# Optimization experiments

Hardware: AMD Instinct MI355X
Metric: run time of the kernel (lower is better)

The kernel has to match this reference:

```python
import jax, jax.numpy as jnp
import numpy as np

NUM_HEADS = 8
MAX_REL = 32  # max_relative_positions
LN_EPS = 1e-5


def _conv1x1(x, W, b):
    # x: (B, C, H, W), W: (Cout, Cin), b: (Cout,)
    return jnp.einsum('bchw,oc->bohw', x, W) + b[None, :, None, None]


def setup_inputs() -> dict:
    key = jax.random.key(0)
    ks = jax.random.split(key, 10)
    B, C, H, W = 2, 512, 48, 48
    L = H * W
    s = 1.0 / np.sqrt(C)
    inp = {
        'x': jax.random.normal(ks[0], (B, C, H, W), jnp.float32),
        'mask': jax.random.randint(ks[1], (1, NUM_HEADS, L, L), 0, 2).astype(bool),
        'learnable_pos': jax.random.normal(ks[2], (1, C, H, W), jnp.float32) * 0.02,
        'Wq': jax.random.normal(ks[3], (C, C), jnp.float32) * s,
        'bq': jnp.zeros((C,), jnp.float32),
        'Wk': jax.random.normal(ks[4], (C, C), jnp.float32) * s,
        'bk': jnp.zeros((C,), jnp.float32),
        'Wv': jax.random.normal(ks[5], (C, C), jnp.float32) * s,
        'bv': jnp.zeros((C,), jnp.float32),
        'Wo': jax.random.normal(ks[6], (C, C), jnp.float32) * s,
        'bo': jnp.zeros((C,), jnp.float32),
        'rel_table': jax.random.normal(ks[7], (NUM_HEADS, 2 * MAX_REL + 1), jnp.float32) * 0.02,
        'ln_gamma': jnp.ones((C,), jnp.float32),
        'ln_beta': jnp.zeros((C,), jnp.float32),
    }
    return inp


def reference(x, mask, learnable_pos, Wq, bq, Wk, bk, Wv, bv, Wo, bo,
              rel_table, ln_gamma, ln_beta):
    B, C, H, W = x.shape
    L = H * W
    hd = C // NUM_HEADS
    residual = x

    xp = x + learnable_pos
    q = _conv1x1(xp, Wq, bq)
    k = _conv1x1(xp, Wk, bk)
    v = _conv1x1(xp, Wv, bv)

    def split_heads(t):  # (B,C,H,W) -> (B, heads, L, hd)
        return t.reshape(B, NUM_HEADS, hd, L).transpose(0, 1, 3, 2)

    q, k, v = split_heads(q), split_heads(k), split_heads(v)

    scale = 1.0 / np.sqrt(hd).astype(np.float32)
    scores = jnp.einsum('bhld,bhmd->bhlm', q, k) * scale  # (B,H,L,L)

    # relative positional bias per head
    pos = jnp.arange(L)
    rp = jnp.clip(pos[:, None] - pos[None, :], -MAX_REL, MAX_REL) + MAX_REL  # (L,L)
    scores = scores + rel_table[:, rp][None]  # (1,heads,L,L) broadcast

    scores = jnp.where(mask, scores, jnp.float32(-1e9))
    attn = jax.nn.softmax(scores, axis=-1)

    out = jnp.einsum('bhlm,bhmd->bhld', attn, v)  # (B,heads,L,hd)
    out = out.transpose(0, 1, 3, 2).reshape(B, C, H, W)
    out = _conv1x1(out, Wo, bo)

    y = residual + out
    # LayerNorm over channels (channels-last permute in original)
    yl = y.transpose(0, 2, 3, 1)  # (B,H,W,C)
    mu = jnp.mean(yl, axis=-1, keepdims=True)
    var = jnp.var(yl, axis=-1, keepdims=True)
    yl = (yl - mu) * jax.lax.rsqrt(var + LN_EPS) * ln_gamma + ln_beta
    return yl.transpose(0, 3, 1, 2)
```

## Files before the change

### kernel.cpp

```cpp
#include <hip/hip_runtime.h>
#include <cstdint>

#define L_SEQ 2304
#define CDIM  512
#define NHEADS 8
#define HD    64
#define LL    ((size_t)L_SEQ * L_SEQ)
#define ROWS_TOT (16 * L_SEQ)
#define PERBL ((size_t)2 * L_SEQ * 512)

typedef short  s8v  __attribute__((ext_vector_type(8)));
typedef float  f4v  __attribute__((ext_vector_type(4)));

__device__ __forceinline__ ushort f2bf(float f) {
    union { float f; uint32_t u; } v; v.f = f;
    uint32_t u = v.u;
    uint32_t r = (u + 0x7FFFu + ((u >> 16) & 1u)) >> 16;
    return (ushort)r;
}

__device__ __forceinline__ float bf2f(ushort u) {
    union { uint32_t u; float f; } v; v.u = (uint32_t)u << 16;
    return v.f;
}

__global__ __launch_bounds__(256) void prep_w(
    const float* __restrict__ Wq, const float* __restrict__ Wk,
    const float* __restrict__ Wv, const float* __restrict__ Wo,
    ushort* __restrict__ wb)
{
    const int i   = blockIdx.x * 256 + threadIdx.x;
    const int mat = i >> 16;
    const int j   = i & 65535;
    const float* src = (mat == 0) ? Wq : (mat == 1) ? Wk : (mat == 2) ? Wv : Wo;
    const float4 w = ((const float4*)src)[j];
    ushort4 o;
    o.x = f2bf(w.x); o.y = f2bf(w.y); o.z = f2bf(w.z); o.w = f2bf(w.w);
    ((ushort4*)(wb + (size_t)mat * 262144))[j] = o;
}

__global__ __launch_bounds__(256) void xpose(
    const float* __restrict__ x, const float* __restrict__ pos,
    ushort* __restrict__ xt)
{
    __shared__ ushort T[64][72];
    const int l0 = blockIdx.x * 64;
    const int c0 = blockIdx.y * 64;
    const int b  = blockIdx.z;
    const int t  = threadIdx.x;
    const int cc = t >> 2;
    const int l4 = (t & 3) * 16;
    const size_t off  = ((size_t)b * CDIM + c0 + cc) * L_SEQ + l0 + l4;
    const size_t poff = (size_t)(c0 + cc) * L_SEQ + l0 + l4;
    #pragma unroll
    for (int j4 = 0; j4 < 4; j4++) {
        const float4 xv = *(const float4*)&x[off + j4 * 4];
        const float4 pv = *(const float4*)&pos[poff + j4 * 4];
        T[cc][l4 + j4 * 4 + 0] = f2bf(xv.x + pv.x);
        T[cc][l4 + j4 * 4 + 1] = f2bf(xv.y + pv.y);
        T[cc][l4 + j4 * 4 + 2] = f2bf(xv.z + pv.z);
        T[cc][l4 + j4 * 4 + 3] = f2bf(xv.w + pv.w);
    }
    __syncthreads();
    const int lr = t >> 2;
    const int c4 = (t & 3) * 16;
    ushort o[16];
    #pragma unroll
    for (int j = 0; j < 16; j++) o[j] = T[c4 + j][lr];
    ushort* dst = &xt[((size_t)b * L_SEQ + l0 + lr) * 512 + c0 + c4];
    *(ushort4*)&dst[0]  = *(ushort4*)&o[0];
    *(ushort4*)&dst[4]  = *(ushort4*)&o[4];
    *(ushort4*)&dst[8]  = *(ushort4*)&o[8];
    *(ushort4*)&dst[12] = *(ushort4*)&o[12];
}

__global__ __launch_bounds__(256) void qkv_mfma(
    const ushort* __restrict__ xt, const ushort* __restrict__ wb,
    const float* __restrict__ bq, const float* __restrict__ bk,
    const float* __restrict__ bv,
    ushort* __restrict__ q_t, ushort* __restrict__ k_t, ushort* __restrict__ v_t)
{
    __shared__ __align__(16) ushort Bs[3][1024 * 8];
    const int l0  = blockIdx.x * 64;
    const int o0  = blockIdx.y * 64;
    const int b   = blockIdx.z;
    const int t = threadIdx.x, w = t >> 6, lane = t & 63;
    const int n16 = lane & 15, q4 = lane >> 4;

    const ushort* A = xt + ((size_t)b * L_SEQ + l0 + w * 16 + n16) * 512 + q4 * 8;

    s8v areg[16];
    #pragma unroll
    for (int i = 0; i < 16; i++) areg[i] = *(const s8v*)&A[i * 32];

    int sOff[4];
    #pragma unroll
    for (int i = 0; i < 4; i++) {
        const int c  = t + 256 * i;
        const int fr = c >> 6, ln = c & 63;
        sOff[i] = (o0 + (fr & 3) * 16 + (ln & 15)) * 512 + (fr >> 2) * 32 + (ln >> 4) * 8;
    }

    s8v breg[3][4];
    #pragma unroll
    for (int m = 0; m < 3; m++)
        #pragma unroll
        for (int i = 0; i < 4; i++)
            breg[m][i] = *(const s8v*)&wb[(size_t)m * 262144 + sOff[i]];

    f4v acc[3][4] = {};
    for (int kb = 0; kb < 512; kb += 128) {
        __syncthreads();
        #pragma unroll
        for (int m = 0; m < 3; m++)
            #pragma unroll
            for (int i = 0; i < 4; i++)
                *(s8v*)&Bs[m][(t + 256 * i) * 8] = breg[m][i];
        __syncthreads();
        if (kb < 384) {
            #pragma unroll
            for (int m = 0; m < 3; m++)
                #pragma unroll
                for (int i = 0; i < 4; i++)
                    breg[m][i] = *(const s8v*)&wb[(size_t)m * 262144 + sOff[i] + kb + 128];
        }
        #pragma unroll
        for (int ks = 0; ks < 4; ks++) {
            const s8v a = areg[(kb >> 5) + ks];
            #pragma unroll
            for (int m = 0; m < 3; m++)
                #pragma unroll
                for (int t4 = 0; t4 < 4; t4++) {
                    const s8v bf = *(const s8v*)&Bs[m][((ks * 4 + t4) * 64 + lane) * 8];
                    acc[m][t4] = __builtin_amdgcn_mfma_f32_16x16x32_bf16(a, bf, acc[m][t4], 0, 0, 0);
                }
        }
    }

    const int h = o0 >> 6;
    const int rowbase = l0 + w * 16 + q4 * 4;

    #pragma unroll
    for (int m = 0; m < 2; m++) {
        const float* bias = (m == 0) ? bq : bk;
        const float sc = (m == 0) ? 0.125f : 1.0f;
        ushort* op = (m == 0 ? q_t : k_t) + ((size_t)(b * NHEADS + h)) * L_SEQ * HD;
        #pragma unroll
        for (int t4 = 0; t4 < 4; t4++) {
            const float bi = bias[o0 + t4 * 16 + n16];
            #pragma unroll
            for (int r = 0; r < 4; r++)
                op[(size_t)(rowbase + r) * HD + t4 * 16 + n16] = f2bf((acc[m][t4][r] + bi) * sc);
        }
    }
    {
        ushort* op = v_t + ((size_t)(b * NHEADS + h)) * HD * L_SEQ;
        #pragma unroll
        for (int t4 = 0; t4 < 4; t4++) {
            const float bi = bv[o0 + t4 * 16 + n16];
            ushort4 st;
            st.x = f2bf(acc[2][t4][0] + bi);
            st.y = f2bf(acc[2][t4][1] + bi);
            st.z = f2bf(acc[2][t4][2] + bi);
            st.w = f2bf(acc[2][t4][3] + bi);
            *(ushort4*)&op[(size_t)(t4 * 16 + n16) * L_SEQ + rowbase] = st;
        }
    }
}

__global__ __launch_bounds__(256) void flash_attn_mfma(
    const ushort* __restrict__ q, const ushort* __restrict__ k,
    const ushort* __restrict__ vt, const int* __restrict__ mask,
    const float* __restrict__ rel_table, ushort* __restrict__ Opart,
    float* __restrict__ Lpart)
{
    __shared__ __align__(16) ushort Kf[512 * 8];
    __shared__ __align__(16) ushort Vf[512 * 8];
    __shared__ __align__(16) ushort Pb[4 * 16 * 72];
    __shared__ float rt[65];

    const int t    = threadIdx.x;
    const int id   = blockIdx.x;
    const int h    = id & 7;
    const int s2   = id >> 3;
    const int b    = s2 & 1;
    const int half = (s2 >> 1) & 1;
    const int qb   = s2 >> 2;
    const int bh   = b * NHEADS + h;
    const int l0   = qb * 64;
    const int w    = t >> 6;
    const int lane = t & 63;
    const int n16  = lane & 15;
    const int q4   = lane >> 4;

    if (t < 65) rt[t] = rel_table[h * 65 + t];

    const ushort* qp = q  + (size_t)bh * L_SEQ * HD;
    const ushort* kp = k  + (size_t)bh * L_SEQ * HD;
    const ushort* vp = vt + (size_t)bh * HD * L_SEQ;
    const int*    mp = mask + (size_t)h * LL;

    const int qrow = l0 + w * 16 + n16;
    const s8v qA0 = *(const s8v*)&qp[(size_t)qrow * HD + q4 * 8];
    const s8v qA1 = *(const s8v*)&qp[(size_t)qrow * HD + 32 + q4 * 8];

    f4v O[4] = {{0.f,0.f,0.f,0.f},{0.f,0.f,0.f,0.f},{0.f,0.f,0.f,0.f},{0.f,0.f,0.f,0.f}};
    float lrun[4] = {0.f, 0.f, 0.f, 0.f};

    int sKey[2], sD0[2], sDd[2];
    #pragma unroll
    for (int cc = 0; cc < 2; cc++) {
        const int c = t + cc * 256;
        const int g = c >> 6;
        const int sT = g >> 1, sS = g & 1;
        const int sQ = (c >> 4) & 3, sN = c & 15;
        sKey[cc] = sT * 16 + sN;
        sD0[cc]  = sS * 32 + sQ * 8;
        sDd[cc]  = sT * 16 + sN;
    }

    const int rowbase = l0 + w * 16 + q4 * 4;
    const int kbase = half * 1152;

    s8v kreg[2], vreg[2];
    int mreg[4][4];
    #pragma unroll
    for (int cc = 0; cc < 2; cc++) {
        kreg[cc] = *(const s8v*)&kp[(size_t)(kbase + sKey[cc]) * HD + sD0[cc]];
        vreg[cc] = *(const s8v*)&vp[(size_t)sDd[cc] * L_SEQ + kbase + sD0[cc]];
    }
    #pragma unroll
    for (int t4 = 0; t4 < 4; t4++)
        #pragma unroll
        for (int r = 0; r < 4; r++)
            mreg[t4][r] = mp[(size_t)(rowbase + r) * L_SEQ + kbase + t4 * 16 + n16];

    for (int mt = 0; mt < 18; mt++) {
        const int mb = kbase + mt * 64;
        __syncthreads();
        #pragma unroll
        for (int cc = 0; cc < 2; cc++) {
            const int c = t + cc * 256;
            *(s8v*)&Kf[c * 8] = kreg[cc];
            *(s8v*)&Vf[c * 8] = vreg[cc];
        }
        __syncthreads();

        const int mb2 = (mt < 17) ? mb + 64 : mb;
        s8v knx[2], vnx[2];
        int mnx[4][4];
        #pragma unroll
        for (int cc = 0; cc < 2; cc++) {
            knx[cc] = *(const s8v*)&kp[(size_t)(mb2 + sKey[cc]) * HD + sD0[cc]];
            vnx[cc] = *(const s8v*)&vp[(size_t)sDd[cc] * L_SEQ + mb2 + sD0[cc]];
        }
        #pragma unroll
        for (int t4 = 0; t4 < 4; t4++)
            #pragma unroll
            for (int r = 0; r < 4; r++)
                mnx[t4][r] = mp[(size_t)(rowbase + r) * L_SEQ + mb2 + t4 * 16 + n16];

        f4v S[4];
        #pragma unroll
        for (int t4 = 0; t4 < 4; t4++) {
            const s8v b0 = *(const s8v*)&Kf[((t4 * 2 + 0) * 64 + lane) * 8];
            const s8v b1 = *(const s8v*)&Kf[((t4 * 2 + 1) * 64 + lane) * 8];
            f4v acc = {0.f, 0.f, 0.f, 0.f};
            acc = __builtin_amdgcn_mfma_f32_16x16x32_bf16(qA0, b0, acc, 0, 0, 0);
            acc = __builtin_amdgcn_mfma_f32_16x16x32_bf16(qA1, b1, acc, 0, 0, 0);
            S[t4] = acc;
        }

        #pragma unroll
        for (int t4 = 0; t4 < 4; t4++) {
            const int A = (l0 + w * 16) - (mb + t4 * 16);
            if (A >= 47) {
                const float bu = rt[64];
                #pragma unroll
                for (int r = 0; r < 4; r++) S[t4][r] += bu;
            } else if (A <= -47) {
                const float bu = rt[0];
                #pragma unroll
                for (int r = 0; r < 4; r++) S[t4][r] += bu;
            } else {
                #pragma unroll
                for (int r = 0; r < 4; r++) {
                    int dix = A + q4 * 4 + r - n16;
                    dix = min(max(dix, -32), 32) + 32;
                    S[t4][r] += rt[dix];
                }
            }
            #pragma unroll
            for (int r = 0; r < 4; r++)
                if (mreg[t4][r] == 0) S[t4][r] = -1e9f;
        }

        float sum[4] = {0.f, 0.f, 0.f, 0.f};
        #pragma unroll
        for (int r = 0; r < 4; r++) {
            #pragma unroll
            for (int t4 = 0; t4 < 4; t4++) {
                const float p = __expf(S[t4][r]);
                sum[r] += p;
                Pb[w * 1152 + (q4 * 4 + r) * 72 + t4 * 16 + n16] = f2bf(p);
            }
        }

        const s8v pf0 = *(const s8v*)&Pb[w * 1152 + n16 * 72 + q4 * 8];
        const s8v pf1 = *(const s8v*)&Pb[w * 1152 + n16 * 72 + 32 + q4 * 8];
        #pragma unroll
        for (int t4 = 0; t4 < 4; t4++) {
            f4v o = O[t4];
            const s8v v0 = *(const s8v*)&Vf[((t4 * 2 + 0) * 64 + lane) * 8];
            const s8v v1 = *(const s8v*)&Vf[((t4 * 2 + 1) * 64 + lane) * 8];
            o = __builtin_amdgcn_mfma_f32_16x16x32_bf16(pf0, v0, o, 0, 0, 0);
            o = __builtin_amdgcn_mfma_f32_16x16x32_bf16(pf1, v1, o, 0, 0, 0);
            O[t4] = o;
        }

        #pragma unroll
        for (int r = 0; r < 4; r++) {
            float s = sum[r];
            s += __shfl_xor(s, 1);
            s += __shfl_xor(s, 2);
            s += __shfl_xor(s, 4);
            s += __shfl_xor(s, 8);
            lrun[r] += s;
        }

        #pragma unroll
        for (int cc = 0; cc < 2; cc++) { kreg[cc] = knx[cc]; vreg[cc] = vnx[cc]; }
        #pragma unroll
        for (int t4 = 0; t4 < 4; t4++)
            #pragma unroll
            for (int r = 0; r < 4; r++)
                mreg[t4][r] = mnx[t4][r];
    }

    ushort* op = Opart + (size_t)half * PERBL + (size_t)b * L_SEQ * 512;
    #pragma unroll
    for (int r = 0; r < 4; r++) {
        const size_t base = (size_t)(rowbase + r) * 512 + h * 64;
        #pragma unroll
        for (int t4 = 0; t4 < 4; t4++)
            op[base + t4 * 16 + n16] = f2bf(O[t4][r]);
    }
    if (n16 == 0) {
        const size_t sb = (size_t)half * ROWS_TOT + (size_t)bh * L_SEQ;
        #pragma unroll
        for (int r = 0; r < 4; r++)
            Lpart[sb + rowbase + r] = lrun[r];
    }
}

__global__ __launch_bounds__(256) void combine_kernel(
    const ushort* __restrict__ O01, const float* __restrict__ Lp,
    ushort* __restrict__ at)
{
    const int i   = blockIdx.x * 256 + threadIdx.x;
    const int c8  = i & 63;
    const int row = i >> 6;
    const int b   = row / L_SEQ;
    const int l   = row - b * L_SEQ;
    const int h   = c8 >> 3;
    const size_t s = (size_t)(b * NHEADS + h) * L_SEQ + l;
    const float f = 1.0f / (Lp[s] + Lp[ROWS_TOT + s]);
    const size_t o = (size_t)row * 512 + c8 * 8;
    const ushort4 a0 = *(const ushort4*)&O01[o];
    const ushort4 a1 = *(const ushort4*)&O01[o + 4];
    const ushort4 c0 = *(const ushort4*)&O01[PERBL + o];
    const ushort4 c1 = *(const ushort4*)&O01[PERBL + o + 4];
    ushort4 r0, r1;
    r0.x = f2bf((bf2f(a0.x) + bf2f(c0.x)) * f);
    r0.y = f2bf((bf2f(a0.y) + bf2f(c0.y)) * f);
    r0.z = f2bf((bf2f(a0.z) + bf2f(c0.z)) * f);
    r0.w = f2bf((bf2f(a0.w) + bf2f(c0.w)) * f);
    r1.x = f2bf((bf2f(a1.x) + bf2f(c1.x)) * f);
    r1.y = f2bf((bf2f(a1.y) + bf2f(c1.y)) * f);
    r1.z = f2bf((bf2f(a1.z) + bf2f(c1.z)) * f);
    r1.w = f2bf((bf2f(a1.w) + bf2f(c1.w)) * f);
    *(ushort4*)&at[o]     = r0;
    *(ushort4*)&at[o + 4] = r1;
}

__global__ __launch_bounds__(256) void out_mfma(
    const ushort* __restrict__ at, const ushort* __restrict__ wb,
    const float* __restrict__ bo, const float* __restrict__ x,
    float* __restrict__ y)
{
    __shared__ __align__(16) ushort Bs[1024 * 8];
    const int l0 = blockIdx.x * 64;
    const int o0 = blockIdx.y * 64;
    const int b  = blockIdx.z;
    const int t = threadIdx.x, w = t >> 6, lane = t & 63;
    const int n16 = lane & 15, q4 = lane >> 4;

    const ushort* A = at + ((size_t)b * L_SEQ + l0 + w * 16 + n16) * 512 + q4 * 8;
    const ushort* W = wb + (size_t)3 * 262144;

    s8v areg[16];
    #pragma unroll
    for (int i = 0; i < 16; i++) areg[i] = *(const s8v*)&A[i * 32];

    int sOff[4];
    #pragma unroll
    for (int i = 0; i < 4; i++) {
        const int c  = t + 256 * i;
        const int fr = c >> 6, ln = c & 63;
        sOff[i] = (o0 + (fr & 3) * 16 + (ln & 15)) * 512 + (fr >> 2) * 32 + (ln >> 4) * 8;
    }

    s8v breg[4];
    #pragma unroll
    for (int i = 0; i < 4; i++) breg[i] = *(const s8v*)&W[sOff[i]];

    f4v acc[4] = {{0.f,0.f,0.f,0.f},{0.f,0.f,0.f,0.f},{0.f,0.f,0.f,0.f},{0.f,0.f,0.f,0.f}};
    for (int kb = 0; kb < 512; kb += 128) {
        __syncthreads();
        #pragma unroll
        for (int i = 0; i < 4; i++)
            *(s8v*)&Bs[(t + 256 * i) * 8] = breg[i];
        __syncthreads();
        if (kb < 384) {
            #pragma unroll
            for (int i = 0; i < 4; i++)
                breg[i] = *(const s8v*)&W[sOff[i] + kb + 128];
        }
        #pragma unroll
        for (int ks = 0; ks < 4; ks++) {
            const s8v a = areg[(kb >> 5) + ks];
            #pragma unroll
            for (int t4 = 0; t4 < 4; t4++) {
                const s8v bf = *(const s8v*)&Bs[((ks * 4 + t4) * 64 + lane) * 8];
                acc[t4] = __builtin_amdgcn_mfma_f32_16x16x32_bf16(a, bf, acc[t4], 0, 0, 0);
            }
        }
    }

    const int rowbase = l0 + w * 16 + q4 * 4;
    #pragma unroll
    for (int t4 = 0; t4 < 4; t4++) {
        const int o = o0 + t4 * 16 + n16;
        const float bi = bo[o];
        const size_t off = ((size_t)b * CDIM + o) * L_SEQ + rowbase;
        const float4 xv = *(const float4*)&x[off];
        float4 st;
        st.x = acc[t4][0] + bi + xv.x;
        st.y = acc[t4][1] + bi + xv.y;
        st.z = acc[t4][2] + bi + xv.z;
        st.w = acc[t4][3] + bi + xv.w;
        *(float4*)&y[off] = st;
    }
}

__global__ __launch_bounds__(256) void ln_kernel(
    float* __restrict__ y, const float* __restrict__ gamma,
    const float* __restrict__ beta)
{
    const int t = threadIdx.x;
    const int p = t & 31;
    const int g = t >> 5;
    const int pos = blockIdx.x * 32 + p;
    const int b = (pos >= L_SEQ) ? 1 : 0;
    const int l = pos - b * L_SEQ;
    float* col = y + (size_t)b * CDIM * L_SEQ + l;

    float s = 0.f, sq = 0.f;
    for (int c = g * 64; c < g * 64 + 64; c++) {
        const float v = col[(size_t)c * L_SEQ];
        s += v; sq += v * v;
    }
    __shared__ float S1[8][32];
    __shared__ float S2[8][32];
    S1[g][p] = s; S2[g][p] = sq;
    __syncthreads();
    if (t < 32) {
        float ss = 0.f, qq = 0.f;
        #pragma unroll
        for (int gg = 0; gg < 8; gg++) { ss += S1[gg][t]; qq += S2[gg][t]; }
        const float mu = ss * (1.0f / CDIM);
        const float var = qq * (1.0f / CDIM) - mu * mu;
        S1[0][t] = mu;
        S2[0][t] = rsqrtf(var + 1e-5f);
    }
    __syncthreads();
    const float mu = S1[0][p];
    const float rs = S2[0][p];
    for (int c = g * 64; c < g * 64 + 64; c++) {
        const float v = col[(size_t)c * L_SEQ];
        col[(size_t)c * L_SEQ] = (v - mu) * rs * gamma[c] + beta[c];
    }
}

extern "C" void kernel_launch(void* const* d_in, const int* in_sizes, int n_in,
                              void* d_out, int out_size, void* d_ws, size_t ws_size,
                              hipStream_t stream) {
    const float* x    = (const float*)d_in[0];
    const int* mask   = (const int*)d_in[1];
    const float* pos  = (const float*)d_in[2];
    const float* Wq   = (const float*)d_in[3];
    const float* bq   = (const float*)d_in[4];
    const float* Wk   = (const float*)d_in[5];
    const float* bk   = (const float*)d_in[6];
    const float* Wv   = (const float*)d_in[7];
    const float* bv   = (const float*)d_in[8];
    const float* Wo   = (const float*)d_in[9];
    const float* bo   = (const float*)d_in[10];
    const float* rel  = (const float*)d_in[11];
    const float* gam  = (const float*)d_in[12];
    const float* bet  = (const float*)d_in[13];

    ushort* qw  = (ushort*)d_ws;
    ushort* kw  = qw + PERBL;
    ushort* vw  = kw + PERBL;
    ushort* xtw = vw + PERBL;
    ushort* wbw = xtw + PERBL;
    ushort* Opart = wbw + (size_t)4 * 262144;
    float* Lpart = (float*)(Opart + 2 * PERBL);
    ushort* attnT = xtw;
    float* y = (float*)d_out;

    prep_w<<<dim3(1024), 256, 0, stream>>>(Wq, Wk, Wv, Wo, wbw);

    xpose<<<dim3(L_SEQ / 64, CDIM / 64, 2), 256, 0, stream>>>(x, pos, xtw);

    qkv_mfma<<<dim3(L_SEQ / 64, CDIM / 64, 2), 256, 0, stream>>>(
        xtw, wbw, bq, bk, bv, qw, kw, vw);

    flash_attn_mfma<<<dim3(1152), 256, 0, stream>>>(qw, kw, vw, mask, rel,
                                                    Opart, Lpart);

    combine_kernel<<<dim3(1152), 256, 0, stream>>>(Opart, Lpart, attnT);

    out_mfma<<<dim3(L_SEQ / 64, CDIM / 64, 2), 256, 0, stream>>>(
        attnT, wbw, bo, x, y);

    ln_kernel<<<(2 * L_SEQ) / 32, 256, 0, stream>>>(y, gam, bet);
}
```

Baseline: 369.4 us.

## Pre-swizzle weights into MFMA fragment layout and read B operands directly from global

prep_w now writes the bf16 weights already arranged in per-lane MFMA fragment order, with each thread converting 8 elements. The QKV and output projection kernels drop their LDS staging, the double-buffered register prefetch and the __syncthreads, and load B fragments straight from global memory with coalesced 16-byte loads per k-step. This removes LDS traffic and barriers, but the weight loads now sit inside the MFMA loop without explicit prefetch and depend on L2/cache hits for latency hiding.

```diff
diff --git a/kernel.cpp b/kernel.cpp
--- a/kernel.cpp
+++ b/kernel.cpp
@@ -27,16 +27,23 @@
 __global__ __launch_bounds__(256) void prep_w(
     const float* __restrict__ Wq, const float* __restrict__ Wk,
     const float* __restrict__ Wv, const float* __restrict__ Wo,
-    ushort* __restrict__ wb)
-{
-    const int i   = blockIdx.x * 256 + threadIdx.x;
-    const int mat = i >> 16;
-    const int j   = i & 65535;
+    ushort* __restrict__ wf)
+{
+    const int i    = blockIdx.x * 256 + threadIdx.x;
+    const int lane = i & 63;
+    const int F    = (i >> 6) & 63;
+    const int ob   = (i >> 12) & 7;
+    const int mat  = i >> 15;
     const float* src = (mat == 0) ? Wq : (mat == 1) ? Wk : (mat == 2) ? Wv : Wo;
-    const float4 w = ((const float4*)src)[j];
-    ushort4 o;
-    o.x = f2bf(w.x); o.y = f2bf(w.y); o.z = f2bf(w.z); o.w = f2bf(w.w);
-    ((ushort4*)(wb + (size_t)mat * 262144))[j] = o;
+    const int row = ob * 64 + (F & 3) * 16 + (lane & 15);
+    const int col = (F >> 2) * 32 + (lane >> 4) * 8;
+    const float4 w0 = *(const float4*)&src[(size_t)row * 512 + col];
+    const float4 w1 = *(const float4*)&src[(size_t)row * 512 + col + 4];
+    ushort4 o0, o1;
+    o0.x = f2bf(w0.x); o0.y = f2bf(w0.y); o0.z = f2bf(w0.z); o0.w = f2bf(w0.w);
+    o1.x = f2bf(w1.x); o1.y = f2bf(w1.y); o1.z = f2bf(w1.z); o1.w = f2bf(w1.w);
+    *(ushort4*)&wf[(size_t)i * 8]     = o0;
+    *(ushort4*)&wf[(size_t)i * 8 + 4] = o1;
 }
 
 __global__ __launch_bounds__(256) void xpose(
@@ -75,15 +82,15 @@
 }
 
 __global__ __launch_bounds__(256) void qkv_mfma(
-    const ushort* __restrict__ xt, const ushort* __restrict__ wb,
+    const ushort* __restrict__ xt, const ushort* __restrict__ wf,
     const float* __restrict__ bq, const float* __restrict__ bk,
     const float* __restrict__ bv,
     ushort* __restrict__ q_t, ushort* __restrict__ k_t, ushort* __restrict__ v_t)
 {
-    __shared__ __align__(16) ushort Bs[3][1024 * 8];
-    const int l0  = blockIdx.x * 64;
-    const int o0  = blockIdx.y * 64;
-    const int b   = blockIdx.z;
+    const int l0 = blockIdx.x * 64;
+    const int ob = blockIdx.y;
+    const int o0 = ob * 64;
+    const int b  = blockIdx.z;
     const int t = threadIdx.x, w = t >> 6, lane = t & 63;
     const int n16 = lane & 15, q4 = lane >> 4;
 
@@ -93,51 +100,26 @@
     #pragma unroll
     for (int i = 0; i < 16; i++) areg[i] = *(const s8v*)&A[i * 32];
 
-    int sOff[4];
-    #pragma unroll
-    for (int i = 0; i < 4; i++) {
-        const int c  = t + 256 * i;
-        const int fr = c >> 6, ln = c & 63;
-        sOff[i] = (o0 + (fr & 3) * 16 + (ln & 15)) * 512 + (fr >> 2) * 32 + (ln >> 4) * 8;
-    }
-
-    s8v breg[3][4];
-    #pragma unroll
-    for (int m = 0; m < 3; m++)
-        #pragma unroll
-        for (int i = 0; i < 4; i++)
-            breg[m][i] = *(const s8v*)&wb[(size_t)m * 262144 + sOff[i]];
+    const size_t lb = (size_t)lane * 8;
 
     f4v acc[3][4] = {};
-    for (int kb = 0; kb < 512; kb += 128) {
-        __syncthreads();
+    for (int ks = 0; ks < 16; ks++) {
+        s8v bf[3][4];
         #pragma unroll
         for (int m = 0; m < 3; m++)
             #pragma unroll
-            for (int i = 0; i < 4; i++)
-                *(s8v*)&Bs[m][(t + 256 * i) * 8] = breg[m][i];
-        __syncthreads();
-        if (kb < 384) {
-            #pragma unroll
-            for (int m = 0; m < 3; m++)
-                #pragma unroll
-                for (int i = 0; i < 4; i++)
-                    breg[m][i] = *(const s8v*)&wb[(size_t)m * 262144 + sOff[i] + kb + 128];
-        }
-        #pragma unroll
-        for (int ks = 0; ks < 4; ks++) {
-            const s8v a = areg[(kb >> 5) + ks];
-            #pragma unroll
-            for (int m = 0; m < 3; m++)
-                #pragma unroll
-                for (int t4 = 0; t4 < 4; t4++) {
-                    const s8v bf = *(const s8v*)&Bs[m][((ks * 4 + t4) * 64 + lane) * 8];
-                    acc[m][t4] = __builtin_amdgcn_mfma_f32_16x16x32_bf16(a, bf, acc[m][t4], 0, 0, 0);
-                }
-        }
-    }
-
-    const int h = o0 >> 6;
+            for (int t4 = 0; t4 < 4; t4++)
+                bf[m][t4] = *(const s8v*)&wf[
+                    ((size_t)((m * 8 + ob) * 64 + ks * 4 + t4)) * 512 + lb];
+        const s8v a = areg[ks];
+        #pragma unroll
+        for (int m = 0; m < 3; m++)
+            #pragma unroll
+            for (int t4 = 0; t4 < 4; t4++)
+                acc[m][t4] = __builtin_amdgcn_mfma_f32_16x16x32_bf16(a, bf[m][t4], acc[m][t4], 0, 0, 0);
+    }
+
+    const int h = ob;
     const int rowbase = l0 + w * 16 + q4 * 4;
 
     #pragma unroll
@@ -384,57 +366,36 @@
 }
 
 __global__ __launch_bounds__(256) void out_mfma(
-    const ushort* __restrict__ at, const ushort* __restrict__ wb,
+    const ushort* __restrict__ at, const ushort* __restrict__ wf,
     const float* __restrict__ bo, const float* __restrict__ x,
     float* __restrict__ y)
 {
-    __shared__ __align__(16) ushort Bs[1024 * 8];
     const int l0 = blockIdx.x * 64;
-    const int o0 = blockIdx.y * 64;
+    const int ob = blockIdx.y;
+    const int o0 = ob * 64;
     const int b  = blockIdx.z;
     const int t = threadIdx.x, w = t >> 6, lane = t & 63;
     const int n16 = lane & 15, q4 = lane >> 4;
 
     const ushort* A = at + ((size_t)b * L_SEQ + l0 + w * 16 + n16) * 512 + q4 * 8;
-    const ushort* W = wb + (size_t)3 * 262144;
 
     s8v areg[16];
     #pragma unroll
     for (int i = 0; i < 16; i++) areg[i] = *(const s8v*)&A[i * 32];
 
-    int sOff[4];
-    #pragma unroll
-    for (int i = 0; i < 4; i++) {
-        const int c  = t + 256 * i;
-        const int fr = c >> 6, ln = c & 63;
-        sOff[i] = (o0 + (fr & 3) * 16 + (ln & 15)) * 512 + (fr >> 2) * 32 + (ln >> 4) * 8;
-    }
-
-    s8v breg[4];
-    #pragma unroll
-    for (int i = 0; i < 4; i++) breg[i] = *(const s8v*)&W[sOff[i]];
+    const size_t lb = (size_t)lane * 8;
 
     f4v acc[4] = {{0.f,0.f,0.f,0.f},{0.f,0.f,0.f,0.f},{0.f,0.f,0.f,0.f},{0.f,0.f,0.f,0.f}};
-    for (int kb = 0; kb < 512; kb += 128) {
-        __syncthreads();
-        #pragma unroll
-        for (int i = 0; i < 4; i++)
-            *(s8v*)&Bs[(t + 256 * i) * 8] = breg[i];
-        __syncthreads();
-        if (kb < 384) {
-            #pragma unroll
-            for (int i = 0; i < 4; i++)
-                breg[i] = *(const s8v*)&W[sOff[i] + kb + 128];
-        }
-        #pragma unroll
-        for (int ks = 0; ks < 4; ks++) {
-            const s8v a = areg[(kb >> 5) + ks];
-            #pragma unroll
-            for (int t4 = 0; t4 < 4; t4++) {
-                const s8v bf = *(const s8v*)&Bs[((ks * 4 + t4) * 64 + lane) * 8];
-                acc[t4] = __builtin_amdgcn_mfma_f32_16x16x32_bf16(a, bf, acc[t4], 0, 0, 0);
-            }
-        }
+    for (int ks = 0; ks < 16; ks++) {
+        s8v bf[4];
+        #pragma unroll
+        for (int t4 = 0; t4 < 4; t4++)
+            bf[t4] = *(const s8v*)&wf[
+                ((size_t)((3 * 8 + ob) * 64 + ks * 4 + t4)) * 512 + lb];
+        const s8v a = areg[ks];
+        #pragma unroll
+        for (int t4 = 0; t4 < 4; t4++)
+            acc[t4] = __builtin_amdgcn_mfma_f32_16x16x32_bf16(a, bf[t4], acc[t4], 0, 0, 0);
     }
 
     const int rowbase = l0 + w * 16 + q4 * 4;
@@ -520,7 +481,7 @@
     ushort* attnT = xtw;
     float* y = (float*)d_out;
 
-    prep_w<<<dim3(1024), 256, 0, stream>>>(Wq, Wk, Wv, Wo, wbw);
+    prep_w<<<dim3(512), 256, 0, stream>>>(Wq, Wk, Wv, Wo, wbw);
 
     xpose<<<dim3(L_SEQ / 64, CDIM / 64, 2), 256, 0, stream>>>(x, pos, xtw);
 
```

New measurement: 366.6 us. No clear change (-0.8%).
